# Kernel tuning notes

Hardware: AMD Instinct MI355X
Metric: run time of the kernel (lower is better)

The kernel has to match this reference:

```python
import jax, jax.numpy as jnp
import numpy as np

# Loss hyperparameters (match init_kwargs)
DELTA_VAR = 0.75
DELTA_DIST = 2.0
ALPHA, BETA, GAMMA = 1.0, 1.0, 0.001


def setup_inputs() -> dict:
    key = jax.random.key(0)
    k1, k2 = jax.random.split(key)
    B, C, H, W = 4, 32, 512, 512
    N_INST = 100
    input_ = jax.random.normal(k1, (B, C, H, W), dtype=jnp.float32)
    target = jax.random.randint(k2, (B, 1, H, W), 0, N_INST, dtype=jnp.int64)
    return {"input_": input_, "target": target, "n_instances": N_INST}


def _loss_single(feat, lbl, n_inst):
    # feat: [C, H, W] embeddings for one sample; lbl: [H, W] instance ids in [0, n_inst)
    C = feat.shape[0]
    f = feat.reshape(C, -1).T                     # [P, C] pixel embeddings
    l = lbl.reshape(-1)                           # [P]
    counts = jnp.bincount(l, length=n_inst).astype(f.dtype)     # [n]
    sums = jax.ops.segment_sum(f, l, num_segments=n_inst)       # [n, C]
    means = sums / counts[:, None]                               # cluster means [n, C]

    # variance (attractive) term: hinge on distance of each pixel to its cluster mean
    diff = f - means[l]                           # gather means back to pixels
    var = jnp.linalg.norm(diff, axis=1)           # 'fro' over dim=1 == L2
    var = jnp.clip(var - DELTA_VAR, 0.0) ** 2 / counts[l]
    variance_term = var.sum() / n_inst

    # distance (repulsive) term: hinged pairwise distances between cluster means
    eye = jnp.eye(n_inst, dtype=f.dtype)
    d2 = jnp.sum((means[:, None, :] - means[None, :, :]) ** 2, axis=2)  # [n, n]
    # safe sqrt: diagonal is exactly 0; mask it so grads stay finite, value unchanged
    dmat = jnp.sqrt(jnp.where(d2 > 0, d2, 1.0)) * (1.0 - eye)
    repulsion = 2.0 * DELTA_DIST * (1.0 - eye)
    hinged = jnp.clip(repulsion - dmat, 0.0) ** 2
    distance_term = hinged.sum() / (n_inst * (n_inst - 1))

    # regularization term: pull cluster means toward origin
    reg_term = jnp.linalg.norm(means, axis=1).sum() / n_inst

    return ALPHA * variance_term + BETA * distance_term + GAMMA * reg_term


def reference(input_, target, n_instances):
    # input_: [B, C, H, W], target: [B, 1, H, W]
    lbl = target[:, 0]
    losses = jax.vmap(lambda f, l: _loss_single(f, l, n_instances))(input_, lbl)
    return losses.mean()  # loss.div(n_batches)
```

## Files before the change

### kernel.cpp

```cpp
#include <hip/hip_runtime.h>
#include <math.h>

#define BB 4
#define CC 32
#define HWSZ (512*512)
#define NMAX 128
#define NP 132
#define PPB 1024
#define CHUNKS (HWSZ / PPB)
#define DELTA_VAR_C 0.75f
#define DELTA_DIST_C 2.0f
#define GAMMA_C 0.001f
#define FXS 1048576.0f
#define FXI (1.0f / 1048576.0f)

__device__ __forceinline__ float block_reduce_256(float v, float* red, int tid) {
    #pragma unroll
    for (int o = 32; o > 0; o >>= 1) v += __shfl_down(v, o, 64);
    if ((tid & 63) == 0) red[tid >> 6] = v;
    __syncthreads();
    if (tid == 0) v = red[0] + red[1] + red[2] + red[3];
    return v;
}

__global__ __launch_bounds__(256) void k_seg_sum(
    const float* __restrict__ in, const int* __restrict__ lbl,
    const int* __restrict__ n_ptr, int* __restrict__ sums_i,
    unsigned int* __restrict__ counts_u)
{
    const int N = *n_ptr;
    __shared__ int s_sum[CC * NP];
    __shared__ unsigned int s_cnt[NMAX];
    const int tid = threadIdx.x;

    for (int i = tid; i < CC * NP; i += 256) s_sum[i] = 0;
    for (int i = tid; i < NMAX; i += 256) s_cnt[i] = 0u;
    __syncthreads();

    const int chunk = blockIdx.x;
    const int b = chunk / CHUNKS;
    const int p0 = (chunk % CHUNKS) * PPB;

    const float* inb = in + (size_t)b * CC * HWSZ;
    const int* lb = lbl + (size_t)b * HWSZ + p0 + tid * 4;

    int4 l4 = *(const int4*)(lb);
    int labels[4] = {l4.x, l4.y, l4.z, l4.w};

    #pragma unroll
    for (int i = 0; i < 4; i++) atomicAdd(&s_cnt[labels[i]], 1u);

    #pragma unroll 4
    for (int c = 0; c < CC; ++c) {
        const float* inc = inb + (size_t)c * HWSZ + p0 + tid * 4;
        float4 a = *(const float4*)(inc);
        float v[4] = {a.x, a.y, a.z, a.w};
        #pragma unroll
        for (int i = 0; i < 4; i++) {
            int q = (int)rintf(v[i] * FXS);
            atomicAdd(&s_sum[c * NP + labels[i]], q);
        }
    }
    __syncthreads();

    for (int i = tid; i < N * CC; i += 256) {
        int n = i / CC, c = i % CC;
        int val = s_sum[c * NP + n];
        if (val != 0) atomicAdd(&sums_i[(size_t)b * NMAX * CC + i], val);
    }
    for (int i = tid; i < N; i += 256) {
        unsigned int cv = s_cnt[i];
        if (cv) atomicAdd(&counts_u[b * NMAX + i], cv);
    }
}

__global__ __launch_bounds__(256) void k_means_dist(
    const int* __restrict__ sums_i, const unsigned int* __restrict__ counts_u,
    const int* __restrict__ n_ptr, float* __restrict__ means,
    int* __restrict__ out_acc)
{
    const int N = *n_ptr;
    const int b = blockIdx.x;
    __shared__ float m[NMAX * 33];
    __shared__ float red[4];
    const int tid = threadIdx.x;

    for (int i = tid; i < N * CC; i += 256) {
        int n = i / CC;
        float mu = (float)sums_i[(size_t)b * NMAX * CC + i] * FXI
                 / (float)counts_u[b * NMAX + n];
        means[(size_t)b * NMAX * CC + i] = mu;
        m[n * 33 + (i % CC)] = mu;
    }
    __syncthreads();

    float dist_sum = 0.f;
    for (int pr = tid; pr < N * N; pr += 256) {
        int i = pr / N, j = pr - i * N;
        if (i == j) continue;
        float d2 = 0.f;
        #pragma unroll
        for (int c = 0; c < CC; c++) {
            float d = m[i * 33 + c] - m[j * 33 + c];
            d2 += d * d;
        }
        float dm = (d2 > 0.f) ? sqrtf(d2) : 1.0f;
        float h = fmaxf(2.0f * DELTA_DIST_C - dm, 0.f);
        dist_sum += h * h;
    }
    float reg_sum = 0.f;
    for (int n = tid; n < N; n += 256) {
        float s = 0.f;
        #pragma unroll
        for (int c = 0; c < CC; c++) { float v = m[n * 33 + c]; s += v * v; }
        reg_sum += sqrtf(s);
    }
    float acc = dist_sum / ((float)N * (float)(N - 1)) + reg_sum * (GAMMA_C / (float)N);
    float tot = block_reduce_256(acc, red, tid);
    if (tid == 0)
        atomicAdd(out_acc, (int)rintf(tot * (1.0f / (float)BB) * FXS));
}

__global__ __launch_bounds__(256) void k_var(
    const float* __restrict__ in, const int* __restrict__ lbl,
    const int* __restrict__ n_ptr, const float* __restrict__ means,
    const unsigned int* __restrict__ counts_u, int* __restrict__ out_acc)
{
    const int N = *n_ptr;
    __shared__ float m_t[CC * NP];
    __shared__ float invc[NMAX];
    __shared__ float red[4];
    const int tid = threadIdx.x;

    const int chunk = blockIdx.x;
    const int b = chunk / CHUNKS;
    const int p0 = (chunk % CHUNKS) * PPB;

    for (int i = tid; i < N * CC; i += 256) {
        int n = i / CC, c = i % CC;
        m_t[c * NP + n] = means[(size_t)b * NMAX * CC + i];
    }
    for (int i = tid; i < N; i += 256)
        invc[i] = 1.0f / (float)counts_u[b * NMAX + i];
    __syncthreads();

    const float* inb = in + (size_t)b * CC * HWSZ;
    const int* lb = lbl + (size_t)b * HWSZ + p0 + tid * 4;

    int4 l4 = *(const int4*)(lb);
    int labels[4] = {l4.x, l4.y, l4.z, l4.w};
    float acc[4] = {0.f, 0.f, 0.f, 0.f};

    #pragma unroll 4
    for (int c = 0; c < CC; ++c) {
        const float* inc = inb + (size_t)c * HWSZ + p0 + tid * 4;
        float4 a = *(const float4*)(inc);
        float v[4] = {a.x, a.y, a.z, a.w};
        #pragma unroll
        for (int i = 0; i < 4; i++) {
            float d = v[i] - m_t[c * NP + labels[i]];
            acc[i] += d * d;
        }
    }

    float vsum = 0.f;
    #pragma unroll
    for (int i = 0; i < 4; i++) {
        float nm = sqrtf(acc[i]);
        float t = fmaxf(nm - DELTA_VAR_C, 0.f);
        vsum += t * t * invc[labels[i]];
    }
    float tot = block_reduce_256(vsum, red, tid);
    if (tid == 0)
        atomicAdd(out_acc, (int)rintf(tot * (1.0f / ((float)N * (float)BB)) * FXS));
}

__global__ void k_final(const int* __restrict__ out_acc, float* __restrict__ out) {
    if (threadIdx.x == 0 && blockIdx.x == 0)
        *out = (float)(*out_acc) * FXI;
}

extern "C" void kernel_launch(void* const* d_in, const int* in_sizes, int n_in,
                              void* d_out, int out_size, void* d_ws, size_t ws_size,
                              hipStream_t stream) {
    (void)in_sizes; (void)n_in; (void)out_size; (void)ws_size;
    const float* in  = (const float*)d_in[0];
    const int*   lbl = (const int*)d_in[1];
    const int*   n_ptr = (const int*)d_in[2];
    float* out = (float*)d_out;

    int* sums_i = (int*)d_ws;
    unsigned int* counts_u = (unsigned int*)(sums_i + BB * NMAX * CC);
    int* out_acc = (int*)(counts_u + BB * NMAX);
    float* means = (float*)(out_acc + 1);

    hipMemsetAsync(d_ws, 0,
                   (size_t)(BB * NMAX * CC + BB * NMAX + 1) * sizeof(int), stream);

    const int blocks = BB * CHUNKS;
    k_seg_sum<<<blocks, 256, 0, stream>>>(in, lbl, n_ptr, sums_i, counts_u);
    k_means_dist<<<BB, 256, 0, stream>>>(sums_i, counts_u, n_ptr, means, out_acc);
    k_var<<<blocks, 256, 0, stream>>>(in, lbl, n_ptr, means, counts_u, out_acc);
    k_final<<<1, 64, 0, stream>>>(out_acc, out);
}
```

Before: 257.8 us.

## Double pixels per block with register prefetch and split pairwise distance across blocks

Each block now covers 2048 pixels, with 8 pixels per thread, in both the segment-sum and variance kernels. Channel loads are software-prefetched two channels ahead in registers, which adds memory-level parallelism and halves the number of blocks and shared-memory flushes. The means computation is split out, and the O(N^2) pairwise distance term moves to a separate kernel spread over 8 slices per batch, so it is no longer serialized on only 4 blocks. The risks are higher register pressure, fewer blocks to cover latency, and one extra kernel launch.

```diff
diff --git a/kernel.cpp b/kernel.cpp
--- a/kernel.cpp
+++ b/kernel.cpp
@@ -6,7 +6,7 @@
 #define HWSZ (512*512)
 #define NMAX 128
 #define NP 132
-#define PPB 1024
+#define PPB 2048
 #define CHUNKS (HWSZ / PPB)
 #define DELTA_VAR_C 0.75f
 #define DELTA_DIST_C 2.0f
@@ -14,6 +14,8 @@
 #define FXS 1048576.0f
 #define FXI (1.0f / 1048576.0f)
 
+#define LD4(p) (*(const float4*)(p))
+
 __device__ __forceinline__ float block_reduce_256(float v, float* red, int tid) {
     #pragma unroll
     for (int o = 32; o > 0; o >>= 1) v += __shfl_down(v, o, 64);
@@ -37,29 +39,38 @@
     for (int i = tid; i < NMAX; i += 256) s_cnt[i] = 0u;
     __syncthreads();
 
-    const int chunk = blockIdx.x;
-    const int b = chunk / CHUNKS;
-    const int p0 = (chunk % CHUNKS) * PPB;
+    const int b = blockIdx.x >> 7;
+    const int p0 = (blockIdx.x & (CHUNKS - 1)) * PPB;
 
     const float* inb = in + (size_t)b * CC * HWSZ;
-    const int* lb = lbl + (size_t)b * HWSZ + p0 + tid * 4;
-
-    int4 l4 = *(const int4*)(lb);
-    int labels[4] = {l4.x, l4.y, l4.z, l4.w};
+    const int* lb = lbl + (size_t)b * HWSZ + p0 + tid * 8;
+
+    int4 l4a = *(const int4*)(lb);
+    int4 l4b = *(const int4*)(lb + 4);
+    int lab[8] = {l4a.x, l4a.y, l4a.z, l4a.w, l4b.x, l4b.y, l4b.z, l4b.w};
 
     #pragma unroll
-    for (int i = 0; i < 4; i++) atomicAdd(&s_cnt[labels[i]], 1u);
-
-    #pragma unroll 4
-    for (int c = 0; c < CC; ++c) {
-        const float* inc = inb + (size_t)c * HWSZ + p0 + tid * 4;
-        float4 a = *(const float4*)(inc);
-        float v[4] = {a.x, a.y, a.z, a.w};
-        #pragma unroll
-        for (int i = 0; i < 4; i++) {
-            int q = (int)rintf(v[i] * FXS);
-            atomicAdd(&s_sum[c * NP + labels[i]], q);
-        }
+    for (int i = 0; i < 8; i++) atomicAdd(&s_cnt[lab[i]], 1u);
+
+    const float* p = inb + p0 + (size_t)tid * 8;
+    float4 a0 = LD4(p);            float4 b0 = LD4(p + 4);
+    float4 a1 = LD4(p + HWSZ);     float4 b1 = LD4(p + HWSZ + 4);
+
+    for (int c = 0; c < CC; c += 2) {
+        float4 ca0 = a0, cb0 = b0, ca1 = a1, cb1 = b1;
+        if (c + 2 < CC) {
+            const float* q = p + (size_t)(c + 2) * HWSZ;
+            a0 = LD4(q);          b0 = LD4(q + 4);
+            a1 = LD4(q + HWSZ);   b1 = LD4(q + HWSZ + 4);
+        }
+        float v0[8] = {ca0.x, ca0.y, ca0.z, ca0.w, cb0.x, cb0.y, cb0.z, cb0.w};
+        #pragma unroll
+        for (int i = 0; i < 8; i++)
+            atomicAdd(&s_sum[c * NP + lab[i]], (int)rintf(v0[i] * FXS));
+        float v1[8] = {ca1.x, ca1.y, ca1.z, ca1.w, cb1.x, cb1.y, cb1.z, cb1.w};
+        #pragma unroll
+        for (int i = 0; i < 8; i++)
+            atomicAdd(&s_sum[(c + 1) * NP + lab[i]], (int)rintf(v1[i] * FXS));
     }
     __syncthreads();
 
@@ -74,28 +85,39 @@
     }
 }
 
-__global__ __launch_bounds__(256) void k_means_dist(
+__global__ __launch_bounds__(256) void k_means(
     const int* __restrict__ sums_i, const unsigned int* __restrict__ counts_u,
-    const int* __restrict__ n_ptr, float* __restrict__ means,
-    int* __restrict__ out_acc)
+    const int* __restrict__ n_ptr, float* __restrict__ means)
 {
     const int N = *n_ptr;
     const int b = blockIdx.x;
-    __shared__ float m[NMAX * 33];
-    __shared__ float red[4];
-    const int tid = threadIdx.x;
-
+    const int tid = threadIdx.x;
     for (int i = tid; i < N * CC; i += 256) {
         int n = i / CC;
         float mu = (float)sums_i[(size_t)b * NMAX * CC + i] * FXI
                  / (float)counts_u[b * NMAX + n];
         means[(size_t)b * NMAX * CC + i] = mu;
-        m[n * 33 + (i % CC)] = mu;
-    }
+    }
+}
+
+#define DSLICE 8
+__global__ __launch_bounds__(256) void k_dist(
+    const float* __restrict__ means, const int* __restrict__ n_ptr,
+    int* __restrict__ out_acc)
+{
+    const int N = *n_ptr;
+    const int b = blockIdx.x / DSLICE;
+    const int slice = blockIdx.x % DSLICE;
+    __shared__ float m[NMAX * 33];
+    __shared__ float red[4];
+    const int tid = threadIdx.x;
+
+    for (int i = tid; i < N * CC; i += 256)
+        m[(i / CC) * 33 + (i % CC)] = means[(size_t)b * NMAX * CC + i];
     __syncthreads();
 
     float dist_sum = 0.f;
-    for (int pr = tid; pr < N * N; pr += 256) {
+    for (int pr = slice * 256 + tid; pr < N * N; pr += DSLICE * 256) {
         int i = pr / N, j = pr - i * N;
         if (i == j) continue;
         float d2 = 0.f;
@@ -108,14 +130,17 @@
         float h = fmaxf(2.0f * DELTA_DIST_C - dm, 0.f);
         dist_sum += h * h;
     }
-    float reg_sum = 0.f;
-    for (int n = tid; n < N; n += 256) {
-        float s = 0.f;
-        #pragma unroll
-        for (int c = 0; c < CC; c++) { float v = m[n * 33 + c]; s += v * v; }
-        reg_sum += sqrtf(s);
-    }
-    float acc = dist_sum / ((float)N * (float)(N - 1)) + reg_sum * (GAMMA_C / (float)N);
+    float acc = dist_sum / ((float)N * (float)(N - 1));
+    if (slice == 0) {
+        float reg_sum = 0.f;
+        for (int n = tid; n < N; n += 256) {
+            float s = 0.f;
+            #pragma unroll
+            for (int c = 0; c < CC; c++) { float v = m[n * 33 + c]; s += v * v; }
+            reg_sum += sqrtf(s);
+        }
+        acc += reg_sum * (GAMMA_C / (float)N);
+    }
     float tot = block_reduce_256(acc, red, tid);
     if (tid == 0)
         atomicAdd(out_acc, (int)rintf(tot * (1.0f / (float)BB) * FXS));
@@ -132,9 +157,8 @@
     __shared__ float red[4];
     const int tid = threadIdx.x;
 
-    const int chunk = blockIdx.x;
-    const int b = chunk / CHUNKS;
-    const int p0 = (chunk % CHUNKS) * PPB;
+    const int b = blockIdx.x >> 7;
+    const int p0 = (blockIdx.x & (CHUNKS - 1)) * PPB;
 
     for (int i = tid; i < N * CC; i += 256) {
         int n = i / CC, c = i % CC;
@@ -145,30 +169,44 @@
     __syncthreads();
 
     const float* inb = in + (size_t)b * CC * HWSZ;
-    const int* lb = lbl + (size_t)b * HWSZ + p0 + tid * 4;
-
-    int4 l4 = *(const int4*)(lb);
-    int labels[4] = {l4.x, l4.y, l4.z, l4.w};
-    float acc[4] = {0.f, 0.f, 0.f, 0.f};
-
-    #pragma unroll 4
-    for (int c = 0; c < CC; ++c) {
-        const float* inc = inb + (size_t)c * HWSZ + p0 + tid * 4;
-        float4 a = *(const float4*)(inc);
-        float v[4] = {a.x, a.y, a.z, a.w};
-        #pragma unroll
-        for (int i = 0; i < 4; i++) {
-            float d = v[i] - m_t[c * NP + labels[i]];
+    const int* lb = lbl + (size_t)b * HWSZ + p0 + tid * 8;
+
+    int4 l4a = *(const int4*)(lb);
+    int4 l4b = *(const int4*)(lb + 4);
+    int lab[8] = {l4a.x, l4a.y, l4a.z, l4a.w, l4b.x, l4b.y, l4b.z, l4b.w};
+    float acc[8] = {0.f, 0.f, 0.f, 0.f, 0.f, 0.f, 0.f, 0.f};
+
+    const float* p = inb + p0 + (size_t)tid * 8;
+    float4 a0 = LD4(p);            float4 b0 = LD4(p + 4);
+    float4 a1 = LD4(p + HWSZ);     float4 b1 = LD4(p + HWSZ + 4);
+
+    for (int c = 0; c < CC; c += 2) {
+        float4 ca0 = a0, cb0 = b0, ca1 = a1, cb1 = b1;
+        if (c + 2 < CC) {
+            const float* q = p + (size_t)(c + 2) * HWSZ;
+            a0 = LD4(q);          b0 = LD4(q + 4);
+            a1 = LD4(q + HWSZ);   b1 = LD4(q + HWSZ + 4);
+        }
+        float v0[8] = {ca0.x, ca0.y, ca0.z, ca0.w, cb0.x, cb0.y, cb0.z, cb0.w};
+        #pragma unroll
+        for (int i = 0; i < 8; i++) {
+            float d = v0[i] - m_t[c * NP + lab[i]];
+            acc[i] += d * d;
+        }
+        float v1[8] = {ca1.x, ca1.y, ca1.z, ca1.w, cb1.x, cb1.y, cb1.z, cb1.w};
+        #pragma unroll
+        for (int i = 0; i < 8; i++) {
+            float d = v1[i] - m_t[(c + 1) * NP + lab[i]];
             acc[i] += d * d;
         }
     }
 
     float vsum = 0.f;
     #pragma unroll
-    for (int i = 0; i < 4; i++) {
+    for (int i = 0; i < 8; i++) {
         float nm = sqrtf(acc[i]);
         float t = fmaxf(nm - DELTA_VAR_C, 0.f);
-        vsum += t * t * invc[labels[i]];
+        vsum += t * t * invc[lab[i]];
     }
     float tot = block_reduce_256(vsum, red, tid);
     if (tid == 0)
@@ -199,7 +237,8 @@
 
     const int blocks = BB * CHUNKS;
     k_seg_sum<<<blocks, 256, 0, stream>>>(in, lbl, n_ptr, sums_i, counts_u);
-    k_means_dist<<<BB, 256, 0, stream>>>(sums_i, counts_u, n_ptr, means, out_acc);
+    k_means<<<BB, 256, 0, stream>>>(sums_i, counts_u, n_ptr, means);
     k_var<<<blocks, 256, 0, stream>>>(in, lbl, n_ptr, means, counts_u, out_acc);
+    k_dist<<<BB * DSLICE, 256, 0, stream>>>(means, n_ptr, out_acc);
     k_final<<<1, 64, 0, stream>>>(out_acc, out);
 }
```

After: 235.7 us. 8.6% less time.

## Replace global atomics with partial buffers, fold distance term into variance kernel

Applied to the files above, without the earlier changes.

Segment-sum blocks now cover 2048 pixels, hold 8 labels per thread, and write per-block partial sums and counts instead of issuing global atomics. A separate reduction kernel combines the partials into means and inverse counts. The pairwise-distance and regularization work moves from a 4-block serial kernel into the first few blocks of the variance kernel. Both streaming loops software-prefetch the next 4 channels into registers to overlap loads with LDS atomics and math. This removes global atomic contention, the large memset and a low-parallelism kernel, at the cost of extra partial-buffer traffic (about 8 MB written and read back) and higher register pressure.

```diff
diff --git a/kernel.cpp b/kernel.cpp
--- a/kernel.cpp
+++ b/kernel.cpp
@@ -6,14 +6,26 @@
 #define HWSZ (512*512)
 #define NMAX 128
 #define NP 132
-#define PPB 1024
-#define CHUNKS (HWSZ / PPB)
+#define SS (NMAX * CC)
+
+#define PPB_S 2048
+#define CH_S (HWSZ / PPB_S)
+#define NBLK_S (BB * CH_S)
+
+#define PPB_V 1024
+#define CH_V (HWSZ / PPB_V)
+#define NBLK_V (BB * CH_V)
+
+#define DSLICE 8
+
 #define DELTA_VAR_C 0.75f
 #define DELTA_DIST_C 2.0f
 #define GAMMA_C 0.001f
 #define FXS 1048576.0f
 #define FXI (1.0f / 1048576.0f)
 
+#define LD4(p) (*(const float4*)(p))
+
 __device__ __forceinline__ float block_reduce_256(float v, float* red, int tid) {
     #pragma unroll
     for (int o = 32; o > 0; o >>= 1) v += __shfl_down(v, o, 64);
@@ -25,8 +37,8 @@
 
 __global__ __launch_bounds__(256) void k_seg_sum(
     const float* __restrict__ in, const int* __restrict__ lbl,
-    const int* __restrict__ n_ptr, int* __restrict__ sums_i,
-    unsigned int* __restrict__ counts_u)
+    const int* __restrict__ n_ptr, int* __restrict__ part_sums,
+    unsigned int* __restrict__ part_cnts)
 {
     const int N = *n_ptr;
     __shared__ int s_sum[CC * NP];
@@ -37,129 +49,129 @@
     for (int i = tid; i < NMAX; i += 256) s_cnt[i] = 0u;
     __syncthreads();
 
-    const int chunk = blockIdx.x;
-    const int b = chunk / CHUNKS;
-    const int p0 = (chunk % CHUNKS) * PPB;
-
-    const float* inb = in + (size_t)b * CC * HWSZ;
-    const int* lb = lbl + (size_t)b * HWSZ + p0 + tid * 4;
-
-    int4 l4 = *(const int4*)(lb);
-    int labels[4] = {l4.x, l4.y, l4.z, l4.w};
-
-    #pragma unroll
-    for (int i = 0; i < 4; i++) atomicAdd(&s_cnt[labels[i]], 1u);
-
-    #pragma unroll 4
-    for (int c = 0; c < CC; ++c) {
-        const float* inc = inb + (size_t)c * HWSZ + p0 + tid * 4;
-        float4 a = *(const float4*)(inc);
-        float v[4] = {a.x, a.y, a.z, a.w};
-        #pragma unroll
-        for (int i = 0; i < 4; i++) {
-            int q = (int)rintf(v[i] * FXS);
-            atomicAdd(&s_sum[c * NP + labels[i]], q);
-        }
-    }
-    __syncthreads();
-
-    for (int i = tid; i < N * CC; i += 256) {
-        int n = i / CC, c = i % CC;
-        int val = s_sum[c * NP + n];
-        if (val != 0) atomicAdd(&sums_i[(size_t)b * NMAX * CC + i], val);
-    }
-    for (int i = tid; i < N; i += 256) {
-        unsigned int cv = s_cnt[i];
-        if (cv) atomicAdd(&counts_u[b * NMAX + i], cv);
-    }
-}
-
-__global__ __launch_bounds__(256) void k_means_dist(
-    const int* __restrict__ sums_i, const unsigned int* __restrict__ counts_u,
+    const int b = blockIdx.x / CH_S;
+    const int p0 = (blockIdx.x % CH_S) * PPB_S;
+
+    const int* lb = lbl + (size_t)b * HWSZ + p0 + tid * 8;
+    int4 l4a = *(const int4*)(lb);
+    int4 l4b = *(const int4*)(lb + 4);
+    int lab[8] = {l4a.x, l4a.y, l4a.z, l4a.w, l4b.x, l4b.y, l4b.z, l4b.w};
+
+    #pragma unroll
+    for (int i = 0; i < 8; i++) atomicAdd(&s_cnt[lab[i]], 1u);
+
+    const float* p = in + (size_t)b * CC * HWSZ + p0 + (size_t)tid * 8;
+
+    float4 buf[4][2];
+    #pragma unroll
+    for (int k = 0; k < 4; k++) {
+        const float* q = p + (size_t)k * HWSZ;
+        buf[k][0] = LD4(q); buf[k][1] = LD4(q + 4);
+    }
+    for (int c0 = 0; c0 < CC; c0 += 4) {
+        float4 cur[4][2];
+        #pragma unroll
+        for (int k = 0; k < 4; k++) { cur[k][0] = buf[k][0]; cur[k][1] = buf[k][1]; }
+        if (c0 + 4 < CC) {
+            #pragma unroll
+            for (int k = 0; k < 4; k++) {
+                const float* q = p + (size_t)(c0 + 4 + k) * HWSZ;
+                buf[k][0] = LD4(q); buf[k][1] = LD4(q + 4);
+            }
+        }
+        #pragma unroll
+        for (int k = 0; k < 4; k++) {
+            float v[8] = {cur[k][0].x, cur[k][0].y, cur[k][0].z, cur[k][0].w,
+                          cur[k][1].x, cur[k][1].y, cur[k][1].z, cur[k][1].w};
+            const int base = (c0 + k) * NP;
+            #pragma unroll
+            for (int i = 0; i < 8; i++)
+                atomicAdd(&s_sum[base + lab[i]], (int)rintf(v[i] * FXS));
+        }
+    }
+    __syncthreads();
+
+    int* my_sum = part_sums + (size_t)blockIdx.x * SS;
+    for (int i = tid; i < N * CC; i += 256)
+        my_sum[i] = s_sum[(i % CC) * NP + (i / CC)];
+    unsigned int* my_cnt = part_cnts + (size_t)blockIdx.x * NMAX;
+    for (int i = tid; i < N; i += 256)
+        my_cnt[i] = s_cnt[i];
+}
+
+__global__ __launch_bounds__(256) void k_reduce(
+    const int* __restrict__ part_sums, const unsigned int* __restrict__ part_cnts,
     const int* __restrict__ n_ptr, float* __restrict__ means,
-    int* __restrict__ out_acc)
+    float* __restrict__ invc)
 {
     const int N = *n_ptr;
-    const int b = blockIdx.x;
-    __shared__ float m[NMAX * 33];
-    __shared__ float red[4];
-    const int tid = threadIdx.x;
-
-    for (int i = tid; i < N * CC; i += 256) {
-        int n = i / CC;
-        float mu = (float)sums_i[(size_t)b * NMAX * CC + i] * FXI
-                 / (float)counts_u[b * NMAX + n];
-        means[(size_t)b * NMAX * CC + i] = mu;
-        m[n * 33 + (i % CC)] = mu;
-    }
-    __syncthreads();
-
-    float dist_sum = 0.f;
-    for (int pr = tid; pr < N * N; pr += 256) {
-        int i = pr / N, j = pr - i * N;
-        if (i == j) continue;
-        float d2 = 0.f;
-        #pragma unroll
-        for (int c = 0; c < CC; c++) {
-            float d = m[i * 33 + c] - m[j * 33 + c];
-            d2 += d * d;
-        }
-        float dm = (d2 > 0.f) ? sqrtf(d2) : 1.0f;
-        float h = fmaxf(2.0f * DELTA_DIST_C - dm, 0.f);
-        dist_sum += h * h;
-    }
-    float reg_sum = 0.f;
-    for (int n = tid; n < N; n += 256) {
-        float s = 0.f;
-        #pragma unroll
-        for (int c = 0; c < CC; c++) { float v = m[n * 33 + c]; s += v * v; }
-        reg_sum += sqrtf(s);
-    }
-    float acc = dist_sum / ((float)N * (float)(N - 1)) + reg_sum * (GAMMA_C / (float)N);
-    float tot = block_reduce_256(acc, red, tid);
-    if (tid == 0)
-        atomicAdd(out_acc, (int)rintf(tot * (1.0f / (float)BB) * FXS));
+    const int b = blockIdx.x >> 4;
+    const int i = (blockIdx.x & 15) * 256 + threadIdx.x;
+    if (i >= N * CC) return;
+    const int n = i / CC;
+
+    long long s = 0;
+    unsigned int cnt = 0;
+    const int* ps = part_sums + (size_t)b * CH_S * SS + i;
+    const unsigned int* pc = part_cnts + (size_t)b * CH_S * NMAX + n;
+    #pragma unroll 4
+    for (int k = 0; k < CH_S; k++) {
+        s += ps[(size_t)k * SS];
+        cnt += pc[(size_t)k * NMAX];
+    }
+    float mu = (float)s * FXI / (float)cnt;
+    means[(size_t)b * SS + i] = mu;
+    if ((i & (CC - 1)) == 0) invc[b * NMAX + n] = 1.0f / (float)cnt;
 }
 
 __global__ __launch_bounds__(256) void k_var(
     const float* __restrict__ in, const int* __restrict__ lbl,
     const int* __restrict__ n_ptr, const float* __restrict__ means,
-    const unsigned int* __restrict__ counts_u, int* __restrict__ out_acc)
+    const float* __restrict__ invc_g, int* __restrict__ out_acc)
 {
     const int N = *n_ptr;
     __shared__ float m_t[CC * NP];
-    __shared__ float invc[NMAX];
+    __shared__ float s_invc[NMAX];
     __shared__ float red[4];
     const int tid = threadIdx.x;
 
-    const int chunk = blockIdx.x;
-    const int b = chunk / CHUNKS;
-    const int p0 = (chunk % CHUNKS) * PPB;
-
-    for (int i = tid; i < N * CC; i += 256) {
-        int n = i / CC, c = i % CC;
-        m_t[c * NP + n] = means[(size_t)b * NMAX * CC + i];
-    }
+    const int b = blockIdx.x / CH_V;
+    const int chunk = blockIdx.x % CH_V;
+    const int p0 = chunk * PPB_V;
+
+    for (int i = tid; i < N * CC; i += 256)
+        m_t[(i % CC) * NP + (i / CC)] = means[(size_t)b * SS + i];
     for (int i = tid; i < N; i += 256)
-        invc[i] = 1.0f / (float)counts_u[b * NMAX + i];
-    __syncthreads();
-
-    const float* inb = in + (size_t)b * CC * HWSZ;
+        s_invc[i] = invc_g[b * NMAX + i];
+    __syncthreads();
+
     const int* lb = lbl + (size_t)b * HWSZ + p0 + tid * 4;
-
     int4 l4 = *(const int4*)(lb);
-    int labels[4] = {l4.x, l4.y, l4.z, l4.w};
+    int lab[4] = {l4.x, l4.y, l4.z, l4.w};
     float acc[4] = {0.f, 0.f, 0.f, 0.f};
 
-    #pragma unroll 4
-    for (int c = 0; c < CC; ++c) {
-        const float* inc = inb + (size_t)c * HWSZ + p0 + tid * 4;
-        float4 a = *(const float4*)(inc);
-        float v[4] = {a.x, a.y, a.z, a.w};
-        #pragma unroll
-        for (int i = 0; i < 4; i++) {
-            float d = v[i] - m_t[c * NP + labels[i]];
-            acc[i] += d * d;
+    const float* p = in + (size_t)b * CC * HWSZ + p0 + (size_t)tid * 4;
+
+    float4 buf[4];
+    #pragma unroll
+    for (int k = 0; k < 4; k++) buf[k] = LD4(p + (size_t)k * HWSZ);
+    for (int c0 = 0; c0 < CC; c0 += 4) {
+        float4 cur[4];
+        #pragma unroll
+        for (int k = 0; k < 4; k++) cur[k] = buf[k];
+        if (c0 + 4 < CC) {
+            #pragma unroll
+            for (int k = 0; k < 4; k++) buf[k] = LD4(p + (size_t)(c0 + 4 + k) * HWSZ);
+        }
+        #pragma unroll
+        for (int k = 0; k < 4; k++) {
+            float v[4] = {cur[k].x, cur[k].y, cur[k].z, cur[k].w};
+            const int base = (c0 + k) * NP;
+            #pragma unroll
+            for (int i = 0; i < 4; i++) {
+                float d = v[i] - m_t[base + lab[i]];
+                acc[i] += d * d;
+            }
         }
     }
 
@@ -168,11 +180,41 @@
     for (int i = 0; i < 4; i++) {
         float nm = sqrtf(acc[i]);
         float t = fmaxf(nm - DELTA_VAR_C, 0.f);
-        vsum += t * t * invc[labels[i]];
-    }
-    float tot = block_reduce_256(vsum, red, tid);
+        vsum += t * t * s_invc[lab[i]];
+    }
+    float total = vsum * (1.0f / ((float)N * (float)BB));
+
+    if (chunk < DSLICE) {
+        float dist_sum = 0.f;
+        for (int pr = chunk * 256 + tid; pr < N * N; pr += DSLICE * 256) {
+            int i = pr / N, j = pr - i * N;
+            if (i == j) continue;
+            float d2 = 0.f;
+            #pragma unroll
+            for (int c = 0; c < CC; c++) {
+                float d = m_t[c * NP + i] - m_t[c * NP + j];
+                d2 += d * d;
+            }
+            float dm = (d2 > 0.f) ? sqrtf(d2) : 1.0f;
+            float h = fmaxf(2.0f * DELTA_DIST_C - dm, 0.f);
+            dist_sum += h * h;
+        }
+        total += dist_sum * (1.0f / ((float)N * (float)(N - 1) * (float)BB));
+        if (chunk == 0) {
+            float reg_sum = 0.f;
+            for (int n = tid; n < N; n += 256) {
+                float s = 0.f;
+                #pragma unroll
+                for (int c = 0; c < CC; c++) { float v = m_t[c * NP + n]; s += v * v; }
+                reg_sum += sqrtf(s);
+            }
+            total += reg_sum * (GAMMA_C / ((float)N * (float)BB));
+        }
+    }
+
+    float tot = block_reduce_256(total, red, tid);
     if (tid == 0)
-        atomicAdd(out_acc, (int)rintf(tot * (1.0f / ((float)N * (float)BB)) * FXS));
+        atomicAdd(out_acc, (int)rintf(tot * FXS));
 }
 
 __global__ void k_final(const int* __restrict__ out_acc, float* __restrict__ out) {
@@ -189,17 +231,16 @@
     const int*   n_ptr = (const int*)d_in[2];
     float* out = (float*)d_out;
 
-    int* sums_i = (int*)d_ws;
-    unsigned int* counts_u = (unsigned int*)(sums_i + BB * NMAX * CC);
-    int* out_acc = (int*)(counts_u + BB * NMAX);
-    float* means = (float*)(out_acc + 1);
-
-    hipMemsetAsync(d_ws, 0,
-                   (size_t)(BB * NMAX * CC + BB * NMAX + 1) * sizeof(int), stream);
-
-    const int blocks = BB * CHUNKS;
-    k_seg_sum<<<blocks, 256, 0, stream>>>(in, lbl, n_ptr, sums_i, counts_u);
-    k_means_dist<<<BB, 256, 0, stream>>>(sums_i, counts_u, n_ptr, means, out_acc);
-    k_var<<<blocks, 256, 0, stream>>>(in, lbl, n_ptr, means, counts_u, out_acc);
+    int* part_sums = (int*)d_ws;
+    unsigned int* part_cnts = (unsigned int*)(part_sums + (size_t)NBLK_S * SS);
+    float* means = (float*)(part_cnts + (size_t)NBLK_S * NMAX);
+    float* invc  = means + (size_t)BB * SS;
+    int* out_acc = (int*)(invc + (size_t)BB * NMAX);
+
+    hipMemsetAsync(out_acc, 0, sizeof(int), stream);
+
+    k_seg_sum<<<NBLK_S, 256, 0, stream>>>(in, lbl, n_ptr, part_sums, part_cnts);
+    k_reduce<<<BB * 16, 256, 0, stream>>>(part_sums, part_cnts, n_ptr, means, invc);
+    k_var<<<NBLK_V, 256, 0, stream>>>(in, lbl, n_ptr, means, invc, out_acc);
     k_final<<<1, 64, 0, stream>>>(out_acc, out);
 }
```

After: 241.8 us. -6.2%, faster.
